# Performance work log

Hardware: AMD Instinct MI355X
Metric: run time of the kernel (lower is better)

## Reference

```python
import jax, jax.numpy as jnp
import numpy as np

VOCAB, EMB, HID = 32000, 512, 1024
B, T = 64, 512


def setup_inputs() -> dict:
    key = jax.random.key(0)
    ks = jax.random.split(key, 8)
    s_ih = 1.0 / np.sqrt(HID)
    return {
        "x": jax.random.randint(ks[0], (B, T), 0, VOCAB),
        "emb": jax.random.normal(ks[1], (VOCAB, EMB), dtype=jnp.float32),
        "W_ih": jax.random.uniform(ks[2], (4 * HID, EMB), minval=-s_ih, maxval=s_ih, dtype=jnp.float32),
        "b_ih": jax.random.uniform(ks[3], (4 * HID,), minval=-s_ih, maxval=s_ih, dtype=jnp.float32),
        "W_hh": jax.random.uniform(ks[4], (4 * HID, HID), minval=-s_ih, maxval=s_ih, dtype=jnp.float32),
        "b_hh": jax.random.uniform(ks[5], (4 * HID,), minval=-s_ih, maxval=s_ih, dtype=jnp.float32),
        "fc_w": jax.random.uniform(ks[6], (HID, HID), minval=-s_ih, maxval=s_ih, dtype=jnp.float32),
        "fc_b": jax.random.uniform(ks[7], (HID,), minval=-s_ih, maxval=s_ih, dtype=jnp.float32),
    }


def reference(x, emb, W_ih, b_ih, W_hh, b_hh, fc_w, fc_b):
    # x: [B, T] int ids -> embedded [T, B, E] (module transposes to time-major)
    e = jnp.swapaxes(emb[x], 0, 1)
    n = x.shape[0]
    hid = W_hh.shape[1]
    # Pre-compute input-to-hidden GEMM for all timesteps at once: [T, B, 4H]
    xg = jnp.einsum("tbe,ge->tbg", e, W_ih) + b_ih

    def step(carry, xt_g):
        h, c = carry
        gates = xt_g + h @ W_hh.T + b_hh  # [B, 4H]
        i, f, g, o = jnp.split(gates, 4, axis=-1)  # torch gate order: i, f, g, o
        c = jax.nn.sigmoid(f) * c + jax.nn.sigmoid(i) * jnp.tanh(g)
        h = jax.nn.sigmoid(o) * jnp.tanh(c)
        return (h, c), None

    h0 = jnp.zeros((n, hid), dtype=e.dtype)
    (h_last, _), _ = jax.lax.scan(step, (h0, h0), xg)
    return h_last @ fc_w.T + fc_b
```

## Files before the change

kernel.cpp:

```cpp
#include <hip/hip_runtime.h>
#include <hip/hip_bf16.h>
#include <stdint.h>

typedef __bf16 bf16_t;
typedef __bf16 bf16x8 __attribute__((ext_vector_type(8)));
typedef float  f32x4  __attribute__((ext_vector_type(4)));
typedef uint32_t u32x4 __attribute__((ext_vector_type(4)));

#define T_STEPS 512
#define BATCH   64
#define EMBD    512
#define HID     1024
#define MROWS   (T_STEPS * BATCH)
#define HSLOT   (BATCH * HID)
#define NBLK    128

#define OFF_FLAGS 0u
#define OFF_RING  32768u
#define OFF_E     (OFF_RING + 262144u)

__global__ __launch_bounds__(256) void k_gather(const int* __restrict__ x,
                                                const float* __restrict__ emb,
                                                bf16_t* __restrict__ e) {
  const int row  = blockIdx.x * 4 + (threadIdx.x >> 6);
  const int lane = threadIdx.x & 63;
  const int t = row >> 6, b = row & 63;
  const int id = x[b * T_STEPS + t];
  const float* src = emb + (size_t)id * EMBD + lane * 8;
  float4 a = *(const float4*)src;
  float4 c = *(const float4*)(src + 4);
  bf16x8 o;
  o[0]=(bf16_t)a.x; o[1]=(bf16_t)a.y; o[2]=(bf16_t)a.z; o[3]=(bf16_t)a.w;
  o[4]=(bf16_t)c.x; o[5]=(bf16_t)c.y; o[6]=(bf16_t)c.z; o[7]=(bf16_t)c.w;
  *(bf16x8*)(e + (size_t)row * EMBD + lane * 8) = o;
}

__global__ __launch_bounds__(512, 1) void k_lstm(const float* __restrict__ Whh,
                                                 const float* __restrict__ Wih,
                                                 const float* __restrict__ bih,
                                                 const float* __restrict__ bhh,
                                                 const bf16_t* __restrict__ e,
                                                 bf16_t* __restrict__ ring,
                                                 int* __restrict__ flags) {
  __shared__ __align__(16) char Ws[65536];
  __shared__ __align__(16) char Wi[32768];
  __shared__ float gb[2][2][64 * 33];
  __shared__ float bsh[32];
  __shared__ bf16_t hstage[512];
  const int tid = threadIdx.x;
  const int lane = tid & 63;
  const int w = tid >> 6;
  const int s = w >> 2;
  const int w4 = w & 3;
  const int bb = blockIdx.x;
  const int l15 = lane & 15, lq = lane >> 4;
  const int nmask = (l15 & 7) << 4;

  for (int c0 = tid; c0 < 4096; c0 += 512) {
    int n = c0 >> 7, koff = c0 & 127;
    int grow = (n >> 3) * HID + bb * 8 + (n & 7);
    const float4* src = (const float4*)(Whh + (size_t)grow * HID + koff * 8);
    float4 a = src[0], b = src[1];
    bf16x8 v;
    v[0]=(bf16_t)a.x; v[1]=(bf16_t)a.y; v[2]=(bf16_t)a.z; v[3]=(bf16_t)a.w;
    v[4]=(bf16_t)b.x; v[5]=(bf16_t)b.y; v[6]=(bf16_t)b.z; v[7]=(bf16_t)b.w;
    *(bf16x8*)(Ws + n * 2048 + ((koff * 16) ^ ((n & 7) << 4))) = v;
  }
  for (int c0 = tid; c0 < 2048; c0 += 512) {
    int n = c0 >> 6, koff = c0 & 63;
    int grow = (n >> 3) * HID + bb * 8 + (n & 7);
    const float4* src = (const float4*)(Wih + (size_t)grow * EMBD + koff * 8);
    float4 a = src[0], b = src[1];
    bf16x8 v;
    v[0]=(bf16_t)a.x; v[1]=(bf16_t)a.y; v[2]=(bf16_t)a.z; v[3]=(bf16_t)a.w;
    v[4]=(bf16_t)b.x; v[5]=(bf16_t)b.y; v[6]=(bf16_t)b.z; v[7]=(bf16_t)b.w;
    *(bf16x8*)(Wi + n * 1024 + ((koff * 16) ^ ((n & 7) << 4))) = v;
  }
  if (tid < 32) {
    int g = (tid >> 3) * HID + bb * 8 + (tid & 7);
    bsh[tid] = bih[g] + bhh[g];
  }
  __syncthreads();

  bf16x8 wb0[16], wb1[16];
  {
    const char* wr0 = Ws + l15 * 2048;
    const char* wr1 = Ws + (16 + l15) * 2048;
    #pragma unroll
    for (int kk = 0; kk < 16; ++kk) {
      int off = ((s * 16 + kk) * 64 + lq * 16) ^ nmask;
      wb0[kk] = *(const bf16x8*)(wr0 + off);
      wb1[kk] = *(const bf16x8*)(wr1 + off);
    }
  }

  float c_st = 0.f;
  const int un = lane & 7;
  const int gbatch = w * 8 + (lane >> 3);
  const int a_row = w4 * 16 + l15;
  const char* wi0 = Wi + l15 * 1024;
  const char* wi1 = Wi + (16 + l15) * 1024;

  for (int t = 0; t < T_STEPS; ++t) {
    const bf16_t* hp = ring + (size_t)(t & 1) * HSLOT;
    bf16_t* hn = ring + (size_t)((t + 1) & 1) * HSLOT;
    const int par = t & 1;

    f32x4 acc0 = {0.f, 0.f, 0.f, 0.f};
    f32x4 acc1 = {0.f, 0.f, 0.f, 0.f};

    {
      const bf16_t* ep = e + ((size_t)t * BATCH + a_row) * EMBD + s * 256 + lq * 8;
      #pragma unroll
      for (int kk = 0; kk < 8; ++kk) {
        bf16x8 a  = *(const bf16x8*)(ep + kk * 32);
        int off = ((s * 8 + kk) * 64 + lq * 16) ^ nmask;
        bf16x8 b0 = *(const bf16x8*)(wi0 + off);
        bf16x8 b1 = *(const bf16x8*)(wi1 + off);
        acc0 = __builtin_amdgcn_mfma_f32_16x16x32_bf16(a, b0, acc0, 0, 0, 0);
        acc1 = __builtin_amdgcn_mfma_f32_16x16x32_bf16(a, b1, acc1, 0, 0, 0);
      }
    }

    if (w == 0 && t > 0) {
      bool done;
      do {
        int c0 = __hip_atomic_load(flags + lane * 64,        __ATOMIC_RELAXED, __HIP_MEMORY_SCOPE_AGENT);
        int c1 = __hip_atomic_load(flags + (64 + lane) * 64, __ATOMIC_RELAXED, __HIP_MEMORY_SCOPE_AGENT);
        done = __all((c0 < c1 ? c0 : c1) >= t);
        if (!done) __builtin_amdgcn_s_sleep(1);
      } while (!done);
    }
    __syncthreads();
    __builtin_amdgcn_sched_barrier(0);

    bf16x8 hv[16];
    const bf16_t* bp = hp + ((size_t)(s * 64 + lq) << 9) + a_row * 8;
    #pragma unroll
    for (int kk = 0; kk < 16; ++kk) {
      const bf16_t* ad = bp + kk * 2048;
      asm volatile("global_load_dwordx4 %0, %1, off sc0 sc1"
                   : "=v"(hv[kk]) : "v"(ad) : "memory");
    }
    asm volatile("s_waitcnt vmcnt(8)" ::: "memory");
    __builtin_amdgcn_sched_barrier(0);
    #pragma unroll
    for (int kk = 0; kk < 8; ++kk) {
      acc0 = __builtin_amdgcn_mfma_f32_16x16x32_bf16(hv[kk], wb0[kk], acc0, 0, 0, 0);
      acc1 = __builtin_amdgcn_mfma_f32_16x16x32_bf16(hv[kk], wb1[kk], acc1, 0, 0, 0);
    }
    asm volatile("s_waitcnt vmcnt(0)" ::: "memory");
    __builtin_amdgcn_sched_barrier(0);
    #pragma unroll
    for (int kk = 8; kk < 16; ++kk) {
      acc0 = __builtin_amdgcn_mfma_f32_16x16x32_bf16(hv[kk], wb0[kk], acc0, 0, 0, 0);
      acc1 = __builtin_amdgcn_mfma_f32_16x16x32_bf16(hv[kk], wb1[kk], acc1, 0, 0, 0);
    }

    #pragma unroll
    for (int r = 0; r < 4; ++r) {
      int brow = (w4 * 16 + lq * 4 + r) * 33;
      gb[par][s][brow + l15]      = acc0[r];
      gb[par][s][brow + 16 + l15] = acc1[r];
    }
    __syncthreads();

    {
      const float* g0 = &gb[par][0][gbatch * 33];
      const float* g1 = &gb[par][1][gbatch * 33];
      float gi = g0[un]      + g1[un]      + bsh[un];
      float gf = g0[8 + un]  + g1[8 + un]  + bsh[8 + un];
      float gg = g0[16 + un] + g1[16 + un] + bsh[16 + un];
      float go = g0[24 + un] + g1[24 + un] + bsh[24 + un];
      float i_ = 1.f / (1.f + __expf(-gi));
      float f_ = 1.f / (1.f + __expf(-gf));
      float g_ = 1.f - 2.f / (1.f + __expf(2.f * gg));
      float o_ = 1.f / (1.f + __expf(-go));
      c_st = f_ * c_st + i_ * g_;
      hstage[tid] = (bf16_t)(o_ * (1.f - 2.f / (1.f + __expf(2.f * c_st))));
    }
    __syncthreads();

    if (w == 0) {
      u32x4 val = *(const u32x4*)(hstage + lane * 8);
      bf16_t* dst = hn + (size_t)bb * 512 + lane * 8;
      asm volatile("global_store_dwordx4 %0, %1, off sc0 sc1"
                   :: "v"(dst), "v"(val) : "memory");
      asm volatile("s_waitcnt vmcnt(0)" ::: "memory");
      if (lane == 0)
        __hip_atomic_store(flags + bb * 64, t + 1,
                           __ATOMIC_RELAXED, __HIP_MEMORY_SCOPE_AGENT);
    }
  }
}

__global__ __launch_bounds__(256) void k_fc(const bf16_t* __restrict__ h,
                                            const float* __restrict__ fcw,
                                            const float* __restrict__ fcb,
                                            float* __restrict__ out) {
  __shared__ float hs[HID];
  const int b = blockIdx.x >> 2, js = blockIdx.x & 3;
  const int tid = threadIdx.x;
  #pragma unroll
  for (int i = 0; i < 4; ++i) {
    int j = tid * 4 + i;
    hs[j] = (float)h[((j >> 3) << 9) + b * 8 + (j & 7)];
  }
  __syncthreads();
  int j = js * 256 + tid;
  const float4* wr = (const float4*)(fcw + (size_t)j * HID);
  float s = 0.f;
  for (int k = 0; k < 256; ++k) {
    float4 wv = wr[k];
    s += hs[k * 4] * wv.x + hs[k * 4 + 1] * wv.y + hs[k * 4 + 2] * wv.z + hs[k * 4 + 3] * wv.w;
  }
  out[b * HID + j] = s + fcb[j];
}

extern "C" void kernel_launch(void* const* d_in, const int* in_sizes, int n_in,
                              void* d_out, int out_size, void* d_ws, size_t ws_size,
                              hipStream_t stream) {
  const int*   x   = (const int*)  d_in[0];
  const float* emb = (const float*)d_in[1];
  const float* Wih = (const float*)d_in[2];
  const float* bih = (const float*)d_in[3];
  const float* Whh = (const float*)d_in[4];
  const float* bhh = (const float*)d_in[5];
  const float* fcw = (const float*)d_in[6];
  const float* fcb = (const float*)d_in[7];
  float* out = (float*)d_out;

  char* ws = (char*)d_ws;
  int*    flags = (int*)   (ws + OFF_FLAGS);
  bf16_t* ring  = (bf16_t*)(ws + OFF_RING);
  bf16_t* e_b   = (bf16_t*)(ws + OFF_E);
  bf16_t* hfin  = ring;

  (void)hipMemsetAsync(ws, 0, OFF_RING + (size_t)HSLOT * sizeof(bf16_t), stream);

  k_gather<<<MROWS / 4, 256, 0, stream>>>(x, emb, e_b);
  k_lstm<<<NBLK, 512, 0, stream>>>(Whh, Wih, bih, bhh, e_b, ring, flags);
  k_fc<<<BATCH * 4, 256, 0, stream>>>(hfin, fcw, fcb, out);
}
```

Measured before the change: 2.385 ms.

## Publish per-wave h slices with per-wave flags, dropping the staging barrier

Each wave now writes its own bf16 h elements straight to global memory and then sets its own per-wave flag, instead of staging h in LDS, adding a block barrier, and having wave 0 store and set a single flag. The poller reads the 8 per-wave flags of each producer block with vector loads and takes their minimum. This removes one __syncthreads and a serial store-plus-wait from the per-step critical path. In exchange it issues narrow 2-byte stores and polls more flag words per step.

New measurement: 2.496 ms. +4.6%, slower.

```diff
diff --git a/kernel.cpp b/kernel.cpp
--- a/kernel.cpp
+++ b/kernel.cpp
@@ -5,7 +5,7 @@
 typedef __bf16 bf16_t;
 typedef __bf16 bf16x8 __attribute__((ext_vector_type(8)));
 typedef float  f32x4  __attribute__((ext_vector_type(4)));
-typedef uint32_t u32x4 __attribute__((ext_vector_type(4)));
+typedef int    i32x4  __attribute__((ext_vector_type(4)));
 
 #define T_STEPS 512
 #define BATCH   64
@@ -18,6 +18,8 @@
 #define OFF_FLAGS 0u
 #define OFF_RING  32768u
 #define OFF_E     (OFF_RING + 262144u)
+
+__device__ __forceinline__ int imin(int a, int b) { return a < b ? a : b; }
 
 __global__ __launch_bounds__(256) void k_gather(const int* __restrict__ x,
                                                 const float* __restrict__ emb,
@@ -46,7 +48,6 @@
   __shared__ __align__(16) char Wi[32768];
   __shared__ float gb[2][2][64 * 33];
   __shared__ float bsh[32];
-  __shared__ bf16_t hstage[512];
   const int tid = threadIdx.x;
   const int lane = tid & 63;
   const int w = tid >> 6;
@@ -100,6 +101,8 @@
   const int a_row = w4 * 16 + l15;
   const char* wi0 = Wi + l15 * 1024;
   const char* wi1 = Wi + (16 + l15) * 1024;
+  const int* f0p = flags + lane * 64;
+  const int* f1p = flags + (64 + lane) * 64;
 
   for (int t = 0; t < T_STEPS; ++t) {
     const bf16_t* hp = ring + (size_t)(t & 1) * HSLOT;
@@ -125,9 +128,17 @@
     if (w == 0 && t > 0) {
       bool done;
       do {
-        int c0 = __hip_atomic_load(flags + lane * 64,        __ATOMIC_RELAXED, __HIP_MEMORY_SCOPE_AGENT);
-        int c1 = __hip_atomic_load(flags + (64 + lane) * 64, __ATOMIC_RELAXED, __HIP_MEMORY_SCOPE_AGENT);
-        done = __all((c0 < c1 ? c0 : c1) >= t);
+        i32x4 a, b, c, d;
+        asm volatile("global_load_dwordx4 %0, %1, off sc0 sc1"           : "=v"(a) : "v"(f0p) : "memory");
+        asm volatile("global_load_dwordx4 %0, %1, off offset:16 sc0 sc1" : "=v"(b) : "v"(f0p) : "memory");
+        asm volatile("global_load_dwordx4 %0, %1, off sc0 sc1"           : "=v"(c) : "v"(f1p) : "memory");
+        asm volatile("global_load_dwordx4 %0, %1, off offset:16 sc0 sc1" : "=v"(d) : "v"(f1p) : "memory");
+        asm volatile("s_waitcnt vmcnt(0)" ::: "memory");
+        int m0 = imin(imin(imin(a[0], a[1]), imin(a[2], a[3])),
+                      imin(imin(b[0], b[1]), imin(b[2], b[3])));
+        int m1 = imin(imin(imin(c[0], c[1]), imin(c[2], c[3])),
+                      imin(imin(d[0], d[1]), imin(d[2], d[3])));
+        done = __all(imin(m0, m1) >= t);
         if (!done) __builtin_amdgcn_s_sleep(1);
       } while (!done);
     }
@@ -177,19 +188,19 @@
       float g_ = 1.f - 2.f / (1.f + __expf(2.f * gg));
       float o_ = 1.f / (1.f + __expf(-go));
       c_st = f_ * c_st + i_ * g_;
-      hstage[tid] = (bf16_t)(o_ * (1.f - 2.f / (1.f + __expf(2.f * c_st))));
-    }
-    __syncthreads();
-
-    if (w == 0) {
-      u32x4 val = *(const u32x4*)(hstage + lane * 8);
-      bf16_t* dst = hn + (size_t)bb * 512 + lane * 8;
-      asm volatile("global_store_dwordx4 %0, %1, off sc0 sc1"
-                   :: "v"(dst), "v"(val) : "memory");
+      union { bf16_t h; unsigned short u; } pk;
+      pk.h = (bf16_t)(o_ * (1.f - 2.f / (1.f + __expf(2.f * c_st))));
+      unsigned int sval = pk.u;
+      bf16_t* dst = hn + (size_t)bb * 512 + tid;
+      asm volatile("global_store_short %0, %1, off sc0 sc1"
+                   :: "v"(dst), "v"(sval) : "memory");
       asm volatile("s_waitcnt vmcnt(0)" ::: "memory");
-      if (lane == 0)
-        __hip_atomic_store(flags + bb * 64, t + 1,
-                           __ATOMIC_RELAXED, __HIP_MEMORY_SCOPE_AGENT);
+      if (lane == 0) {
+        int fv = t + 1;
+        const int* fdst = flags + bb * 64 + w;
+        asm volatile("global_store_dword %0, %1, off sc0 sc1"
+                     :: "v"(fdst), "v"(fv) : "memory");
+      }
     }
   }
 }
```
